# Optimization experiments

Measured on AMD Instinct MI355X. Metric: run time of the kernel, lower is better.

The kernel has to match this reference:

```python
import jax, jax.numpy as jnp
import numpy as np

NUM_HEADS = 32
NUM_KV_HEADS = 8
HEAD_DIM = 64
ROPE_THETA = 10000.0


def setup_inputs() -> dict:
    key = jax.random.key(0)
    ks = jax.random.split(key, 5)
    B, N, D = 2, 2048, 2048
    kv_out = NUM_KV_HEADS * HEAD_DIM
    s = 0.02
    return {
        "x": jax.random.normal(ks[0], (B, N, D), dtype=jnp.float32),
        "Wq": jax.random.normal(ks[1], (D, D), dtype=jnp.float32) * s,
        "Wk": jax.random.normal(ks[2], (kv_out, D), dtype=jnp.float32) * s,
        "Wv": jax.random.normal(ks[3], (kv_out, D), dtype=jnp.float32) * s,
        "Wo": jax.random.normal(ks[4], (D, D), dtype=jnp.float32) * s,
    }


def _rotate_half(t):
    d = t.shape[-1] // 2
    return jnp.concatenate([-t[..., d:], t[..., :d]], axis=-1)


def _rope_cos_sin(N, dtype):
    # Llama rotary embedding: inv_freq over even dims, duplicated along last axis
    inv_freq = 1.0 / (ROPE_THETA ** (jnp.arange(0, HEAD_DIM, 2, dtype=jnp.float32) / HEAD_DIM))
    freqs = jnp.arange(N, dtype=jnp.float32)[:, None] * inv_freq[None, :]  # [N, hd/2]
    emb = jnp.concatenate([freqs, freqs], axis=-1)  # [N, hd]
    return jnp.cos(emb).astype(dtype), jnp.sin(emb).astype(dtype)


def reference(x, Wq, Wk, Wv, Wo):
    B, N, D = x.shape
    groups = NUM_HEADS // NUM_KV_HEADS
    scale = HEAD_DIM ** -0.5

    q = (x @ Wq.T).reshape(B, N, NUM_HEADS, HEAD_DIM).transpose(0, 2, 1, 3)      # [B,H,N,hd]
    k = (x @ Wk.T).reshape(B, N, NUM_KV_HEADS, HEAD_DIM).transpose(0, 2, 1, 3)   # [B,KVH,N,hd]
    v = (x @ Wv.T).reshape(B, N, NUM_KV_HEADS, HEAD_DIM).transpose(0, 2, 1, 3)

    cos, sin = _rope_cos_sin(N, x.dtype)  # [N,hd]
    cos = cos[None, None]  # [1,1,N,hd]
    sin = sin[None, None]
    q = q * cos + _rotate_half(q) * sin
    k = k * cos + _rotate_half(k) * sin

    # repeat_kv: [B,KVH,N,hd] -> [B,H,N,hd]
    k = jnp.repeat(k, groups, axis=1)
    v = jnp.repeat(v, groups, axis=1)

    attn = jnp.einsum('bhqd,bhkd->bhqk', q, k) * scale  # [B,H,N,N]
    attn = jax.nn.softmax(attn, axis=-1)
    out = jnp.einsum('bhqk,bhkd->bhqd', attn, v)        # [B,H,N,hd]
    out = out.transpose(0, 2, 1, 3).reshape(B, N, D)
    return out @ Wo.T
```

## Files before the change

### kernel.cpp

```cpp
#include <hip/hip_runtime.h>
#include <hip/hip_bf16.h>

#define Bc 2
#define Nc 2048
#define Dc 2048
#define Hc 32
#define KVHc 8

typedef __attribute__((ext_vector_type(4))) float f32x4;
typedef __attribute__((ext_vector_type(8))) short short8;

__device__ __forceinline__ ushort f2b(float f) {
  union { float f; unsigned u; } v; v.f = f;
  unsigned u = v.u;
  unsigned r = (u + 0x7FFFu + ((u >> 16) & 1u)) >> 16;
  return (ushort)r;
}
__device__ __forceinline__ float b2f(ushort h) {
  union { unsigned u; float f; } v; v.u = ((unsigned)h) << 16; return v.f;
}

__device__ __forceinline__ float fexp2(float x) {
  float r;
  asm("v_exp_f32 %0, %1" : "=v"(r) : "v"(x));
  return r;
}

__device__ __forceinline__ unsigned cvt_pk_bf16(float lo, float hi) {
  unsigned r;
  asm("v_cvt_pk_bf16_f32 %0, %1, %2" : "=v"(r) : "v"(lo), "v"(hi));
  return r;
}

__device__ __forceinline__ void gload_lds16(const ushort* g, ushort* l) {
  __builtin_amdgcn_global_load_lds(
      (const __attribute__((address_space(1))) void*)g,
      (__attribute__((address_space(3))) void*)l, 16, 0, 0);
}

template<int ITERS>
__device__ __forceinline__ void stage_tile(const ushort* gbase, int gstride,
                                           ushort* lds, int tid) {
  #pragma unroll
  for (int i = 0; i < ITERS; ++i) {
    int s = i * 256 + tid;
    int row = s >> 3;
    int sch = (s & 7) ^ (row & 7);
    gload_lds16(gbase + (size_t)row * gstride + sch * 8, lds + s * 8);
  }
}
__device__ __forceinline__ short8 read_frag(const ushort* lds, int row, int kbyte) {
  int off = kbyte ^ ((row & 7) << 4);
  return *(const short8*)((const char*)lds + row * 128 + off);
}

__device__ __forceinline__ int f_attn(int row) {
  return ((row >> 1) & 1) | (((row >> 3) & 1) << 1) |
         ((((row >> 2) ^ (row >> 4)) & 1) << 2);
}

__global__ void k_convert_all(
    const float* __restrict__ x,  const float* __restrict__ wq,
    const float* __restrict__ wk, const float* __restrict__ wv,
    const float* __restrict__ wo, ushort* __restrict__ xb,
    ushort* __restrict__ wqkv, ushort* __restrict__ wob) {
  int i = blockIdx.x * 256 + threadIdx.x;
  const float* src; ushort* dst; int off;
  if (i < 2097152)      { src = x;  dst = xb;             off = i; }
  else if (i < 3145728) { src = wq; dst = wqkv;           off = i - 2097152; }
  else if (i < 3407872) { src = wk; dst = wqkv + 4194304; off = i - 3145728; }
  else if (i < 3670016) { src = wv; dst = wqkv + 5242880; off = i - 3407872; }
  else                  { src = wo; dst = wob;            off = i - 3670016; }
  float4 v = ((const float4*)src)[off];
  ushort4 o;
  o.x = f2b(v.x); o.y = f2b(v.y); o.z = f2b(v.z); o.w = f2b(v.w);
  *(ushort4*)&dst[(size_t)off * 4] = o;
}

__global__ void k_rope_table(float* __restrict__ cosT, float* __restrict__ sinT) {
  int i = blockIdx.x * 256 + threadIdx.x;
  int n = i >> 5, f = i & 31;
  float inv = powf(10000.0f, -(float)f * (1.0f / 32.0f));
  float ang = (float)n * inv;
  cosT[i] = cosf(ang);
  sinT[i] = sinf(ang);
}

template<typename TOUT>
__global__ __launch_bounds__(256) void k_gemm_bt(
    const ushort* __restrict__ A, const ushort* __restrict__ Bm,
    TOUT* __restrict__ C, int M, int Nn, int K) {
  __shared__ ushort ldsA[128 * 64];
  __shared__ ushort ldsB[128 * 64];
  int nt = Nn >> 7;
  int m0 = (int)(blockIdx.x / nt) << 7;
  int n0 = (int)(blockIdx.x % nt) << 7;
  int tid = threadIdx.x;
  int lane = tid & 63, w = tid >> 6;
  int wr = w >> 1, wc = w & 1;
  int lc = lane & 15, lq = lane >> 4;
  f32x4 acc[4][4];
  #pragma unroll
  for (int r = 0; r < 4; ++r)
    #pragma unroll
    for (int c = 0; c < 4; ++c) acc[r][c] = (f32x4){0.f, 0.f, 0.f, 0.f};
  int nkt = K >> 6;
  for (int kt = 0; kt < nkt; ++kt) {
    stage_tile<4>(A + (size_t)m0 * K + kt * 64, K, ldsA, tid);
    stage_tile<4>(Bm + (size_t)n0 * K + kt * 64, K, ldsB, tid);
    __syncthreads();
    #pragma unroll
    for (int kk = 0; kk < 2; ++kk) {
      int kbyte = kk * 64 + lq * 16;
      short8 af[4], bfr[4];
      #pragma unroll
      for (int r = 0; r < 4; ++r) af[r] = read_frag(ldsA, wr * 64 + r * 16 + lc, kbyte);
      #pragma unroll
      for (int c = 0; c < 4; ++c) bfr[c] = read_frag(ldsB, wc * 64 + c * 16 + lc, kbyte);
      #pragma unroll
      for (int r = 0; r < 4; ++r)
        #pragma unroll
        for (int c = 0; c < 4; ++c)
          acc[r][c] = __builtin_amdgcn_mfma_f32_16x16x32_bf16(af[r], bfr[c], acc[r][c], 0, 0, 0);
    }
    __syncthreads();
  }
  #pragma unroll
  for (int r = 0; r < 4; ++r)
    #pragma unroll
    for (int c = 0; c < 4; ++c) {
      int gr = m0 + wr * 64 + r * 16 + lq * 4;
      int gc = n0 + wc * 64 + c * 16 + lc;
      #pragma unroll
      for (int e = 0; e < 4; ++e) {
        float val = acc[r][c][e];
        if constexpr (sizeof(TOUT) == 2)
          C[(size_t)(gr + e) * Nn + gc] = f2b(val);
        else
          C[(size_t)(gr + e) * Nn + gc] = val;
      }
    }
}

__global__ void k_rope_qk(const ushort* __restrict__ qkv,
                          const float* __restrict__ cosT, const float* __restrict__ sinT,
                          ushort* __restrict__ qr, ushort* __restrict__ kr) {
  const float QS = 0.125f * 1.44269504089f;
  int bn = blockIdx.x;
  int b = bn >> 11, n = bn & (Nc - 1);
  int t = threadIdx.x;
  const ushort* row = qkv + (size_t)bn * 3072;
  #pragma unroll
  for (int i = 0; i < 4; ++i) {
    int p = i * 256 + t;
    int h = p >> 5, dp = p & 31;
    float c = cosT[n * 32 + dp], s = sinT[n * 32 + dp];
    float q0 = b2f(row[h * 64 + dp]);
    float q1 = b2f(row[h * 64 + dp + 32]);
    size_t ob = ((size_t)(b * Hc + h) * Nc + n) * 64 + dp;
    qr[ob]      = f2b((q0 * c - q1 * s) * QS);
    qr[ob + 32] = f2b((q1 * c + q0 * s) * QS);
  }
  {
    int kvh = t >> 5, dp = t & 31;
    float c = cosT[n * 32 + dp], s = sinT[n * 32 + dp];
    float k0 = b2f(row[2048 + kvh * 64 + dp]);
    float k1 = b2f(row[2048 + kvh * 64 + dp + 32]);
    size_t ob = ((size_t)(b * KVHc + kvh) * Nc + n) * 64 + dp;
    kr[ob]      = f2b(k0 * c - k1 * s);
    kr[ob + 32] = f2b(k1 * c + k0 * s);
  }
}

__global__ void k_transpose_v(const ushort* __restrict__ qkv, ushort* __restrict__ vt) {
  __shared__ ushort tile[64][72];
  int bid = blockIdx.x;
  int ntile = bid & 31, kvh = (bid >> 5) & 7, b = bid >> 8;
  int t = threadIdx.x;
  int n0 = ntile * 64;
  #pragma unroll
  for (int i = 0; i < 4; ++i) {
    int s = i * 256 + t;
    int r = s >> 4, c4 = s & 15;
    ushort4 v = *(const ushort4*)&qkv[(size_t)(b * Nc + n0 + r) * 3072 + 2560 + kvh * 64 + c4 * 4];
    tile[r][c4 * 4 + 0] = v.x; tile[r][c4 * 4 + 1] = v.y;
    tile[r][c4 * 4 + 2] = v.z; tile[r][c4 * 4 + 3] = v.w;
  }
  __syncthreads();
  #pragma unroll
  for (int i = 0; i < 4; ++i) {
    int s = i * 256 + t;
    int d = s >> 4, c4 = s & 15;
    ushort4 v;
    v.x = tile[c4 * 4 + 0][d]; v.y = tile[c4 * 4 + 1][d];
    v.z = tile[c4 * 4 + 2][d]; v.w = tile[c4 * 4 + 3][d];
    *(ushort4*)&vt[(size_t)((b * KVHc + kvh) * 64 + d) * Nc + n0 + c4 * 4] = v;
  }
}

__global__ __launch_bounds__(512) void k_attn(
    const ushort* __restrict__ qr, const ushort* __restrict__ kr,
    const ushort* __restrict__ vt, ushort* __restrict__ ctx) {
  __shared__ ushort ldsK[2][64 * 64];
  __shared__ ushort ldsV[2][64 * 64];
  int bid = blockIdx.x;
  int qt = bid & 31, p = (bid >> 5) & 1, kvh = (bid >> 6) & 7, b = bid >> 9;
  int tid = threadIdx.x;
  int w = tid >> 6, lane = tid & 63;
  int lc = lane & 15, lq = lane >> 4;
  int h = kvh * 4 + p * 2 + (w >> 2);
  int q0 = qt * 64 + (w & 3) * 16;
  const ushort* Qb = qr + (size_t)(b * Hc + h) * Nc * 64;
  const ushort* Kb = kr + (size_t)(b * KVHc + kvh) * Nc * 64;
  const ushort* Vb = vt + (size_t)(b * KVHc + kvh) * 64 * Nc;
  short8 aq[2];
  #pragma unroll
  for (int kk = 0; kk < 2; ++kk)
    aq[kk] = *(const short8*)&Qb[(size_t)(q0 + lc) * 64 + kk * 32 + lq * 8];

  int offK[2][4], offV[2][4];
  #pragma unroll
  for (int c = 0; c < 4; ++c) {
    int rowK = ((c >> 1) << 5) + ((lc >> 2) << 3) + ((c & 1) << 2) + (lc & 3);
    int fs = f_attn(rowK) << 4;
    #pragma unroll
    for (int kk = 0; kk < 2; ++kk)
      offK[kk][c] = rowK * 128 + ((kk * 64 + lq * 16) ^ fs);
  }
  #pragma unroll
  for (int dd = 0; dd < 4; ++dd) {
    int rowV = dd * 16 + lc;
    int fs = f_attn(rowV) << 4;
    #pragma unroll
    for (int kk = 0; kk < 2; ++kk)
      offV[kk][dd] = rowV * 128 + ((kk * 64 + lq * 16) ^ fs);
  }

  int r0 = tid >> 3;
  int c0 = (tid & 7) ^ f_attn(r0);
  int oK0 = r0 * 64 + c0 * 8;
  int oV0 = r0 * Nc + c0 * 8;
  int d0 = tid * 8;

  f32x4 oacc[4];
  #pragma unroll
  for (int d = 0; d < 4; ++d) oacc[d] = (f32x4){0.f, 0.f, 0.f, 0.f};
  float lpart = 0.f;

  auto compute = [&](const ushort* lK, const ushort* lV) {
    f32x4 sc[4];
    __builtin_amdgcn_s_setprio(1);
    #pragma unroll
    for (int c = 0; c < 4; ++c) {
      f32x4 a = (f32x4){0.f, 0.f, 0.f, 0.f};
      #pragma unroll
      for (int kk = 0; kk < 2; ++kk)
        a = __builtin_amdgcn_mfma_f32_16x16x32_bf16(
            *(const short8*)((const char*)lK + offK[kk][c]), aq[kk], a, 0, 0, 0);
      sc[c] = a;
    }
    __builtin_amdgcn_s_setprio(0);
    float ps[4];
    #pragma unroll
    for (int c = 0; c < 4; ++c) {
      #pragma unroll
      for (int e = 0; e < 4; ++e)
        sc[c][e] = fexp2(sc[c][e]);
      ps[c] = (sc[c][0] + sc[c][1]) + (sc[c][2] + sc[c][3]);
    }
    lpart += (ps[0] + ps[1]) + (ps[2] + ps[3]);
    unsigned pk[4][2];
    #pragma unroll
    for (int c = 0; c < 4; ++c) {
      pk[c][0] = cvt_pk_bf16(sc[c][0], sc[c][1]);
      pk[c][1] = cvt_pk_bf16(sc[c][2], sc[c][3]);
    }
    __builtin_amdgcn_s_setprio(1);
    #pragma unroll
    for (int kk = 0; kk < 2; ++kk) {
      union { short8 s; unsigned u[4]; } pa;
      pa.u[0] = pk[2 * kk][0];
      pa.u[1] = pk[2 * kk][1];
      pa.u[2] = pk[2 * kk + 1][0];
      pa.u[3] = pk[2 * kk + 1][1];
      #pragma unroll
      for (int dd = 0; dd < 4; ++dd)
        oacc[dd] = __builtin_amdgcn_mfma_f32_16x16x32_bf16(
            *(const short8*)((const char*)lV + offV[kk][dd]), pa.s, oacc[dd], 0, 0, 0);
    }
    __builtin_amdgcn_s_setprio(0);
  };

  gload_lds16(Kb + oK0, &ldsK[0][d0]);
  gload_lds16(Vb + oV0, &ldsV[0][d0]);
  oK0 += 4096; oV0 += 64;
  __syncthreads();

  constexpr int NT = Nc / 64;
  for (int t2 = 0; t2 < NT; t2 += 2) {
    gload_lds16(Kb + oK0, &ldsK[1][d0]);
    gload_lds16(Vb + oV0, &ldsV[1][d0]);
    oK0 += 4096; oV0 += 64;
    compute(ldsK[0], ldsV[0]);
    __syncthreads();
    if (t2 + 2 < NT) {
      gload_lds16(Kb + oK0, &ldsK[0][d0]);
      gload_lds16(Vb + oV0, &ldsV[0][d0]);
    }
    oK0 += 4096; oV0 += 64;
    compute(ldsK[1], ldsV[1]);
    __syncthreads();
  }
  float lrun = lpart;
  lrun += __shfl_xor(lrun, 16, 64);
  lrun += __shfl_xor(lrun, 32, 64);
  float rinv = 1.f / lrun;
  #pragma unroll
  for (int dd = 0; dd < 4; ++dd) {
    ushort4 o;
    o.x = f2b(oacc[dd][0] * rinv);
    o.y = f2b(oacc[dd][1] * rinv);
    o.z = f2b(oacc[dd][2] * rinv);
    o.w = f2b(oacc[dd][3] * rinv);
    *(ushort4*)&ctx[(size_t)(b * Nc + q0 + lc) * Dc + h * 64 + dd * 16 + lq * 4] = o;
  }
}

extern "C" void kernel_launch(void* const* d_in, const int* in_sizes, int n_in,
                              void* d_out, int out_size, void* d_ws, size_t ws_size,
                              hipStream_t stream) {
  const float* x  = (const float*)d_in[0];
  const float* Wq = (const float*)d_in[1];
  const float* Wk = (const float*)d_in[2];
  const float* Wv = (const float*)d_in[3];
  const float* Wo = (const float*)d_in[4];

  ushort* ws   = (ushort*)d_ws;
  ushort* xb   = ws;
  ushort* wqkv = xb + 8388608;
  ushort* wob  = wqkv + 6291456;
  float*  cosT = (float*)(wob + 4194304);
  float*  sinT = cosT + 65536;
  ushort* qkv  = (ushort*)(sinT + 65536);
  ushort* qr   = qkv + 12582912;
  ushort* kr   = qr + 8388608;
  ushort* vt   = kr + 2097152;
  ushort* ctx  = vt + 2097152;

  k_convert_all<<<18432, 256, 0, stream>>>(x, Wq, Wk, Wv, Wo, xb, wqkv, wob);
  k_rope_table<<<256, 256, 0, stream>>>(cosT, sinT);

  k_gemm_bt<ushort><<<768, 256, 0, stream>>>(xb, wqkv, qkv, 4096, 3072, 2048);
  k_rope_qk<<<4096, 256, 0, stream>>>(qkv, cosT, sinT, qr, kr);
  k_transpose_v<<<512, 256, 0, stream>>>(qkv, vt);
  k_attn<<<1024, 512, 0, stream>>>(qr, kr, vt, ctx);
  k_gemm_bt<float><<<512, 256, 0, stream>>>(ctx, wob, (float*)d_out, 4096, 2048, 2048);
}
```

Baseline: 211.8 us.

## Fuse RoPE and Q/K/V scatter into QKV GEMM epilogue, swizzle block order

The QKV projection GEMM now applies rotary embedding and query scaling in its epilogue, writing rotated Q and K directly in head-major layout and V rows to a compact buffer. This removes the separate RoPE kernel and the round trip of the full QKV intermediate through global memory. Block indices are also remapped in an XCD-style stride-8 swizzle, which may change cache locality. The epilogue does scattered 2-byte stores and per-element cos/sin loads, which may be less coalesced than before.

```diff
diff --git a/kernel.cpp b/kernel.cpp
--- a/kernel.cpp
+++ b/kernel.cpp
@@ -86,15 +86,20 @@
   sinT[i] = sinf(ang);
 }
 
-template<typename TOUT>
+template<int MODE, typename TOUT>
 __global__ __launch_bounds__(256) void k_gemm_bt(
     const ushort* __restrict__ A, const ushort* __restrict__ Bm,
-    TOUT* __restrict__ C, int M, int Nn, int K) {
+    TOUT* __restrict__ C, int M, int Nn, int K,
+    ushort* __restrict__ qro, ushort* __restrict__ kro, ushort* __restrict__ vro,
+    const float* __restrict__ cosT, const float* __restrict__ sinT) {
   __shared__ ushort ldsA[128 * 64];
   __shared__ ushort ldsB[128 * 64];
+  int nwg = gridDim.x;
+  int bid0 = blockIdx.x;
+  int bid = (bid0 & 7) * (nwg >> 3) + (bid0 >> 3);
   int nt = Nn >> 7;
-  int m0 = (int)(blockIdx.x / nt) << 7;
-  int n0 = (int)(blockIdx.x % nt) << 7;
+  int m0 = (bid / nt) << 7;
+  int n0 = (bid % nt) << 7;
   int tid = threadIdx.x;
   int lane = tid & 63, w = tid >> 6;
   int wr = w >> 1, wc = w & 1;
@@ -125,54 +130,77 @@
     }
     __syncthreads();
   }
-  #pragma unroll
-  for (int r = 0; r < 4; ++r)
-    #pragma unroll
-    for (int c = 0; c < 4; ++c) {
-      int gr = m0 + wr * 64 + r * 16 + lq * 4;
-      int gc = n0 + wc * 64 + c * 16 + lc;
-      #pragma unroll
-      for (int e = 0; e < 4; ++e) {
-        float val = acc[r][c][e];
-        if constexpr (sizeof(TOUT) == 2)
-          C[(size_t)(gr + e) * Nn + gc] = f2b(val);
-        else
-          C[(size_t)(gr + e) * Nn + gc] = val;
+  if constexpr (MODE == 0) {
+    #pragma unroll
+    for (int r = 0; r < 4; ++r)
+      #pragma unroll
+      for (int c = 0; c < 4; ++c) {
+        int gr = m0 + wr * 64 + r * 16 + lq * 4;
+        int gc = n0 + wc * 64 + c * 16 + lc;
+        #pragma unroll
+        for (int e = 0; e < 4; ++e) {
+          float val = acc[r][c][e];
+          if constexpr (sizeof(TOUT) == 2)
+            C[(size_t)(gr + e) * Nn + gc] = f2b(val);
+          else
+            C[(size_t)(gr + e) * Nn + gc] = val;
+        }
       }
-    }
-}
-
-__global__ void k_rope_qk(const ushort* __restrict__ qkv,
-                          const float* __restrict__ cosT, const float* __restrict__ sinT,
-                          ushort* __restrict__ qr, ushort* __restrict__ kr) {
-  const float QS = 0.125f * 1.44269504089f;
-  int bn = blockIdx.x;
-  int b = bn >> 11, n = bn & (Nc - 1);
-  int t = threadIdx.x;
-  const ushort* row = qkv + (size_t)bn * 3072;
-  #pragma unroll
-  for (int i = 0; i < 4; ++i) {
-    int p = i * 256 + t;
-    int h = p >> 5, dp = p & 31;
-    float c = cosT[n * 32 + dp], s = sinT[n * 32 + dp];
-    float q0 = b2f(row[h * 64 + dp]);
-    float q1 = b2f(row[h * 64 + dp + 32]);
-    size_t ob = ((size_t)(b * Hc + h) * Nc + n) * 64 + dp;
-    qr[ob]      = f2b((q0 * c - q1 * s) * QS);
-    qr[ob + 32] = f2b((q1 * c + q0 * s) * QS);
-  }
-  {
-    int kvh = t >> 5, dp = t & 31;
-    float c = cosT[n * 32 + dp], s = sinT[n * 32 + dp];
-    float k0 = b2f(row[2048 + kvh * 64 + dp]);
-    float k1 = b2f(row[2048 + kvh * 64 + dp + 32]);
-    size_t ob = ((size_t)(b * KVHc + kvh) * Nc + n) * 64 + dp;
-    kr[ob]      = f2b(k0 * c - k1 * s);
-    kr[ob + 32] = f2b(k1 * c + k0 * s);
-  }
-}
-
-__global__ void k_transpose_v(const ushort* __restrict__ qkv, ushort* __restrict__ vt) {
+  } else {
+    const float QS = 0.125f * 1.44269504089f;
+    int gcB = n0 + wc * 64;
+    if (gcB < 2048) {
+      int hh = gcB >> 6;
+      #pragma unroll
+      for (int r = 0; r < 4; ++r)
+        #pragma unroll
+        for (int e = 0; e < 4; ++e) {
+          int gr = m0 + wr * 64 + r * 16 + lq * 4 + e;
+          int bb = gr >> 11, nn = gr & (Nc - 1);
+          size_t base = ((size_t)((bb * Hc + hh) * Nc + nn)) * 64;
+          #pragma unroll
+          for (int c = 0; c < 2; ++c) {
+            int dp = c * 16 + lc;
+            float co = cosT[nn * 32 + dp], si = sinT[nn * 32 + dp];
+            float v0 = acc[r][c][e], v1 = acc[r][c + 2][e];
+            qro[base + dp]      = f2b((v0 * co - v1 * si) * QS);
+            qro[base + dp + 32] = f2b((v1 * co + v0 * si) * QS);
+          }
+        }
+    } else if (gcB < 2560) {
+      int kvh = (gcB >> 6) - 32;
+      #pragma unroll
+      for (int r = 0; r < 4; ++r)
+        #pragma unroll
+        for (int e = 0; e < 4; ++e) {
+          int gr = m0 + wr * 64 + r * 16 + lq * 4 + e;
+          int bb = gr >> 11, nn = gr & (Nc - 1);
+          size_t base = ((size_t)((bb * KVHc + kvh) * Nc + nn)) * 64;
+          #pragma unroll
+          for (int c = 0; c < 2; ++c) {
+            int dp = c * 16 + lc;
+            float co = cosT[nn * 32 + dp], si = sinT[nn * 32 + dp];
+            float v0 = acc[r][c][e], v1 = acc[r][c + 2][e];
+            kro[base + dp]      = f2b(v0 * co - v1 * si);
+            kro[base + dp + 32] = f2b(v1 * co + v0 * si);
+          }
+        }
+    } else {
+      int vcol = gcB - 2560;
+      #pragma unroll
+      for (int r = 0; r < 4; ++r)
+        #pragma unroll
+        for (int c = 0; c < 4; ++c)
+          #pragma unroll
+          for (int e = 0; e < 4; ++e) {
+            int gr = m0 + wr * 64 + r * 16 + lq * 4 + e;
+            vro[(size_t)gr * 512 + vcol + c * 16 + lc] = f2b(acc[r][c][e]);
+          }
+    }
+  }
+}
+
+__global__ void k_transpose_v(const ushort* __restrict__ vrows, ushort* __restrict__ vt) {
   __shared__ ushort tile[64][72];
   int bid = blockIdx.x;
   int ntile = bid & 31, kvh = (bid >> 5) & 7, b = bid >> 8;
@@ -182,7 +210,7 @@
   for (int i = 0; i < 4; ++i) {
     int s = i * 256 + t;
     int r = s >> 4, c4 = s & 15;
-    ushort4 v = *(const ushort4*)&qkv[(size_t)(b * Nc + n0 + r) * 3072 + 2560 + kvh * 64 + c4 * 4];
+    ushort4 v = *(const ushort4*)&vrows[(size_t)(b * Nc + n0 + r) * 512 + kvh * 64 + c4 * 4];
     tile[r][c4 * 4 + 0] = v.x; tile[r][c4 * 4 + 1] = v.y;
     tile[r][c4 * 4 + 2] = v.z; tile[r][c4 * 4 + 3] = v.w;
   }
@@ -335,24 +363,26 @@
   const float* Wv = (const float*)d_in[3];
   const float* Wo = (const float*)d_in[4];
 
-  ushort* ws   = (ushort*)d_ws;
-  ushort* xb   = ws;
-  ushort* wqkv = xb + 8388608;
-  ushort* wob  = wqkv + 6291456;
-  float*  cosT = (float*)(wob + 4194304);
-  float*  sinT = cosT + 65536;
-  ushort* qkv  = (ushort*)(sinT + 65536);
-  ushort* qr   = qkv + 12582912;
-  ushort* kr   = qr + 8388608;
-  ushort* vt   = kr + 2097152;
-  ushort* ctx  = vt + 2097152;
+  ushort* ws    = (ushort*)d_ws;
+  ushort* xb    = ws;
+  ushort* wqkv  = xb + 8388608;
+  ushort* wob   = wqkv + 6291456;
+  float*  cosT  = (float*)(wob + 4194304);
+  float*  sinT  = cosT + 65536;
+  ushort* vrows = (ushort*)(sinT + 65536);
+  ushort* qr    = vrows + 12582912;
+  ushort* kr    = qr + 8388608;
+  ushort* vt    = kr + 2097152;
+  ushort* ctx   = vt + 2097152;
 
   k_convert_all<<<18432, 256, 0, stream>>>(x, Wq, Wk, Wv, Wo, xb, wqkv, wob);
   k_rope_table<<<256, 256, 0, stream>>>(cosT, sinT);
 
-  k_gemm_bt<ushort><<<768, 256, 0, stream>>>(xb, wqkv, qkv, 4096, 3072, 2048);
-  k_rope_qk<<<4096, 256, 0, stream>>>(qkv, cosT, sinT, qr, kr);
-  k_transpose_v<<<512, 256, 0, stream>>>(qkv, vt);
+  k_gemm_bt<1, ushort><<<768, 256, 0, stream>>>(
+      xb, wqkv, (ushort*)nullptr, 4096, 3072, 2048, qr, kr, vrows, cosT, sinT);
+  k_transpose_v<<<512, 256, 0, stream>>>(vrows, vt);
   k_attn<<<1024, 512, 0, stream>>>(qr, kr, vt, ctx);
-  k_gemm_bt<float><<<512, 256, 0, stream>>>(ctx, wob, (float*)d_out, 4096, 2048, 2048);
-}
+  k_gemm_bt<0, float><<<512, 256, 0, stream>>>(
+      ctx, wob, (float*)d_out, 4096, 2048, 2048,
+      nullptr, nullptr, nullptr, nullptr, nullptr);
+}
```

New measurement: 220.7 us. 1.04x slower.

## Replace QKV projection GEMM with 256x256-tile 8-wave pipelined kernel

Applied to the files above, without the earlier changes.

Adds a new bf16 GEMM for the QKV projection. It uses 256x256 output tiles, 8 waves per block and double-buffered LDS filled by direct global-to-LDS loads with XOR swizzle. The loop interleaves staged loads, barriers and MFMA bursts raised with s_setprio, aiming to hide memory latency and raise MFMA utilisation compared with the old 128x128 kernel. The trade-off is a grid of only 192 blocks with large LDS use, which can leave some CUs idle and limits occupancy.

```diff
diff --git a/kernel.cpp b/kernel.cpp
--- a/kernel.cpp
+++ b/kernel.cpp
@@ -86,6 +86,124 @@
   sinT[i] = sinf(ang);
 }
 
+__global__ __launch_bounds__(512, 2) void k_gemm8(
+    const ushort* __restrict__ A, const ushort* __restrict__ Bm,
+    ushort* __restrict__ C, int M, int Nn, int K) {
+  __shared__ ushort lds[2][2][2][128 * 64];
+  int nt = Nn >> 8;
+  int bid = blockIdx.x;
+  int m0 = (bid / nt) << 8, n0 = (bid % nt) << 8;
+  int tid = threadIdx.x;
+  int lane = tid & 63, w = tid >> 6;
+  int wr = w >> 2, wc = w & 3;
+  int lc = lane & 15, lq = lane >> 4;
+  int nkt = K >> 6, nit = nkt >> 1;
+
+  const ushort* Ag = A + (size_t)m0 * K;
+  const ushort* Bg = Bm + (size_t)n0 * K;
+
+  int r0s = tid >> 3;
+  int sch = (tid & 7) ^ (r0s & 7);
+  size_t g0 = (size_t)r0s * K + sch * 8;
+  size_t g1 = (size_t)(64 + r0s) * K + sch * 8;
+  int l0 = tid * 8, l1 = 4096 + tid * 8;
+
+  int sw = (lc & 7) << 4;
+  int koff0 = (lq * 16) ^ sw;
+  int koff1 = (64 + lq * 16) ^ sw;
+  int abase = lc * 128;
+  int bbase = ((wc & 1) * 64 + lc) * 128;
+
+  f32x4 acc[8][4];
+  #pragma unroll
+  for (int r = 0; r < 8; ++r)
+    #pragma unroll
+    for (int c = 0; c < 4; ++c) acc[r][c] = (f32x4){0.f, 0.f, 0.f, 0.f};
+  short8 afr[4][2], bfr[4][2];
+
+  auto STAGE = [&](int op, int h, int t) {
+    if (t >= nkt) t -= nkt;
+    const ushort* gb = (op ? Bg : Ag) + (size_t)(h * 128) * K + t * 64;
+    ushort* lb = &lds[t & 1][op][h][0];
+    gload_lds16(gb + g0, lb + l0);
+    gload_lds16(gb + g1, lb + l1);
+  };
+  auto LDA = [&](int b, int mh) {
+    const char* p = (const char*)&lds[b][0][wr][0];
+    #pragma unroll
+    for (int mi = 0; mi < 4; ++mi) {
+      int rb = abase + (mh * 4 + mi) * 2048;
+      afr[mi][0] = *(const short8*)(p + rb + koff0);
+      afr[mi][1] = *(const short8*)(p + rb + koff1);
+    }
+  };
+  auto LDB = [&](int b, int nh) {
+    const char* p = (const char*)&lds[b][1][wc >> 1][0];
+    #pragma unroll
+    for (int ni = 0; ni < 2; ++ni) {
+      int rb = bbase + (nh * 2 + ni) * 2048;
+      bfr[nh * 2 + ni][0] = *(const short8*)(p + rb + koff0);
+      bfr[nh * 2 + ni][1] = *(const short8*)(p + rb + koff1);
+    }
+  };
+  auto MFMA16 = [&](int mh, int nh) {
+    __builtin_amdgcn_s_setprio(1);
+    #pragma unroll
+    for (int mi = 0; mi < 4; ++mi)
+      #pragma unroll
+      for (int ni = 0; ni < 2; ++ni) {
+        f32x4 a = acc[mh * 4 + mi][nh * 2 + ni];
+        a = __builtin_amdgcn_mfma_f32_16x16x32_bf16(afr[mi][0], bfr[nh * 2 + ni][0], a, 0, 0, 0);
+        a = __builtin_amdgcn_mfma_f32_16x16x32_bf16(afr[mi][1], bfr[nh * 2 + ni][1], a, 0, 0, 0);
+        acc[mh * 4 + mi][nh * 2 + ni] = a;
+      }
+    __builtin_amdgcn_s_setprio(0);
+  };
+
+  #define BAR __builtin_amdgcn_s_barrier()
+  #define LGK do { asm volatile("s_waitcnt lgkmcnt(0)" ::: "memory"); \
+                   __builtin_amdgcn_sched_barrier(0); } while (0)
+  #define VM4 asm volatile("s_waitcnt vmcnt(4)" ::: "memory")
+
+  STAGE(1, 0, 0); STAGE(0, 0, 0); STAGE(0, 1, 0); STAGE(1, 1, 0);
+  STAGE(1, 0, 1); STAGE(1, 1, 1);
+  VM4; BAR;
+
+  for (int i = 0; i < nit; ++i) {
+    int t1 = 2 * i + 1;
+    LDA(0, 0); LDB(0, 0); STAGE(0, 0, t1);
+    BAR; LGK; MFMA16(0, 0); BAR;
+    LDB(0, 1); STAGE(0, 1, t1);
+    BAR; LGK; MFMA16(0, 1); BAR;
+    LDA(0, 1); STAGE(1, 0, t1 + 1);
+    BAR; LGK; MFMA16(1, 1); BAR;
+    STAGE(0, 0, t1 + 1);
+    BAR; MFMA16(1, 0); VM4; BAR;
+    LDA(1, 0); LDB(1, 0); STAGE(0, 1, t1 + 1);
+    BAR; LGK; MFMA16(0, 0); BAR;
+    LDB(1, 1); STAGE(1, 1, t1 + 1);
+    BAR; LGK; MFMA16(0, 1); BAR;
+    LDA(1, 1); STAGE(1, 0, t1 + 2);
+    BAR; LGK; MFMA16(1, 1); BAR;
+    STAGE(1, 1, t1 + 2);
+    BAR; MFMA16(1, 0); VM4; BAR;
+  }
+  #undef BAR
+  #undef LGK
+  #undef VM4
+
+  #pragma unroll
+  for (int mf = 0; mf < 8; ++mf)
+    #pragma unroll
+    for (int nf = 0; nf < 4; ++nf) {
+      int gr = m0 + wr * 128 + mf * 16 + lq * 4;
+      int gc = n0 + wc * 64 + nf * 16 + lc;
+      #pragma unroll
+      for (int e = 0; e < 4; ++e)
+        C[(size_t)(gr + e) * Nn + gc] = f2b(acc[mf][nf][e]);
+    }
+}
+
 template<typename TOUT>
 __global__ __launch_bounds__(256) void k_gemm_bt(
     const ushort* __restrict__ A, const ushort* __restrict__ Bm,
@@ -350,7 +468,7 @@
   k_convert_all<<<18432, 256, 0, stream>>>(x, Wq, Wk, Wv, Wo, xb, wqkv, wob);
   k_rope_table<<<256, 256, 0, stream>>>(cosT, sinT);
 
-  k_gemm_bt<ushort><<<768, 256, 0, stream>>>(xb, wqkv, qkv, 4096, 3072, 2048);
+  k_gemm8<<<192, 512, 0, stream>>>(xb, wqkv, qkv, 4096, 3072, 2048);
   k_rope_qk<<<4096, 256, 0, stream>>>(qkv, cosT, sinT, qr, kr);
   k_transpose_v<<<512, 256, 0, stream>>>(qkv, vt);
   k_attn<<<1024, 512, 0, stream>>>(qr, kr, vt, ctx);
```

New measurement: 208.8 us. No clear change (-1.5%).
